# Optimization experiments

Measured on AMD Instinct MI355X. Metric: run time of the kernel, lower is better.

## Reference

```python
import jax, jax.numpy as jnp
import numpy as np

B, S, H = 4, 2048, 1024  # batch, seq, hidden


def setup_inputs() -> dict:
    key = jax.random.key(0)
    kq, kk, kv = jax.random.split(key, 3)
    return {
        "Q": jax.random.normal(kq, (B, S, H), dtype=jnp.float32),
        "K": jax.random.normal(kk, (B, S, H), dtype=jnp.float32),
        "V": jax.random.normal(kv, (B, S, H), dtype=jnp.float32),
    }


def reference(Q, K, V):
    # Phase of rfft along hidden dim -> [B, S, F], F = H//2 + 1
    q_fft = jnp.fft.rfft(Q, axis=-1)
    k_fft = jnp.fft.rfft(K, axis=-1)
    q_phase = jnp.arctan2(q_fft.imag, q_fft.real)
    k_phase = jnp.arctan2(k_fft.imag, k_fft.real)
    n_freqs = q_phase.shape[-1]
    # mean_f cos(qp_i - kp_j) = (cos(qp) @ cos(kp)^T + sin(qp) @ sin(kp)^T) / F
    # Avoids materializing the [B,S,S,F] phase_diff tensor; math is identical.
    align = (
        jnp.einsum("bif,bjf->bij", jnp.cos(q_phase), jnp.cos(k_phase))
        + jnp.einsum("bif,bjf->bij", jnp.sin(q_phase), jnp.sin(k_phase))
    ) / n_freqs
    scores = align + 1.0
    weights = jax.nn.softmax(scores, axis=-1)  # [B, S, S]
    output = jnp.einsum("bij,bjh->bih", weights, V)  # [B, S, H]
    return output, weights
```

## Files before the change

### kernel.cpp

```cpp
#include <hip/hip_runtime.h>
#include <hip/hip_bf16.h>
#include <math.h>

#define Bb 4
#define Ss 2048
#define Hh 1024
#define Ff 513
#define FEAT 1026
#define KP2 1088

typedef __attribute__((ext_vector_type(8))) short bf16x8;
typedef __attribute__((ext_vector_type(4))) float f32x4;

typedef const __attribute__((address_space(1))) void GVoid;
typedef __attribute__((address_space(3))) void LVoid;

#define PADI(i) ((i) + ((i) >> 4))

__device__ __forceinline__ float2 cmul(float2 a, float2 b) {
  return make_float2(a.x * b.x - a.y * b.y, a.x * b.y + a.y * b.x);
}

__device__ __forceinline__ unsigned short bf16bits(float x) {
  __hip_bfloat16 h = __float2bfloat16(x);
  return *reinterpret_cast<unsigned short*>(&h);
}

__device__ __forceinline__ bf16x8 lds_read_b128(const short* p) {
  bf16x8 r;
  asm volatile("ds_read_b128 %0, %1"
               : "=&v"(r)
               : "v"((const __attribute__((address_space(3))) short*)p));
  return r;
}

__global__ __launch_bounds__(256) void fft_phase_kernel(
    const float* __restrict__ Q, const float* __restrict__ Kin,
    __hip_bfloat16* __restrict__ FQ, __hip_bfloat16* __restrict__ FK) {
  const int row = blockIdx.x;
  const float* qs = Q   + (size_t)row * Hh;
  const float* ks = Kin + (size_t)row * Hh;
  __hip_bfloat16* fq = FQ + (size_t)row * KP2;
  __hip_bfloat16* fk = FK + (size_t)row * KP2;

  __shared__ float2 data[PADI(1023) + 1];
  __shared__ float2 tw[1024];
  const int tid = threadIdx.x;

#pragma unroll
  for (int e = 0; e < 4; ++e) {
    const int m = tid + e * 256;
    float s, c;
    sincosf(-6.283185307179586f * (float)m * (1.0f / 1024.0f), &s, &c);
    tw[m] = make_float2(c, s);
  }
#pragma unroll
  for (int e = 0; e < 4; ++e) {
    const int n = tid + e * 256;
    const int r4 = ((n & 3) << 8) | (((n >> 2) & 3) << 6) | (((n >> 4) & 3) << 4)
                 | (((n >> 6) & 3) << 2) | ((n >> 8) & 3);
    data[PADI(r4)] = make_float2(qs[n], ks[n]);
  }
  __syncthreads();

  int quarter = 1, step = 256;
  for (int s = 0; s < 5; ++s) {
    const int j = tid & (quarter - 1);
    const int pos = 4 * tid - 3 * j;
    const float2 x0 = data[PADI(pos)];
    const float2 x1 = data[PADI(pos + quarter)];
    const float2 x2 = data[PADI(pos + 2 * quarter)];
    const float2 x3 = data[PADI(pos + 3 * quarter)];
    const int e1 = j * step;
    const float2 a1 = cmul(x1, tw[e1]);
    const float2 a2 = cmul(x2, tw[2 * e1]);
    const float2 a3 = cmul(x3, tw[3 * e1]);
    const float2 t0 = make_float2(x0.x + a2.x, x0.y + a2.y);
    const float2 t1 = make_float2(x0.x - a2.x, x0.y - a2.y);
    const float2 t2 = make_float2(a1.x + a3.x, a1.y + a3.y);
    const float2 t3 = make_float2(a1.x - a3.x, a1.y - a3.y);
    data[PADI(pos)]               = make_float2(t0.x + t2.x, t0.y + t2.y);
    data[PADI(pos + quarter)]     = make_float2(t1.x + t3.y, t1.y - t3.x);
    data[PADI(pos + 2 * quarter)] = make_float2(t0.x - t2.x, t0.y - t2.y);
    data[PADI(pos + 3 * quarter)] = make_float2(t1.x - t3.y, t1.y + t3.x);
    __syncthreads();
    quarter <<= 2; step >>= 2;
  }

  for (int f = tid; f <= 512; f += 256) {
    const float2 z1 = data[PADI(f)];
    const float2 z2 = data[PADI((1024 - f) & 1023)];
    const float qr = z1.x + z2.x, qi = z1.y - z2.y;
    const float kr = z1.y + z2.y, ki = z2.x - z1.x;
    float qc, qsn, kc, ksn;
    const float qm2 = qr * qr + qi * qi;
    if (qm2 > 1e-30f) { const float iv = rsqrtf(qm2); qc = qr * iv; qsn = qi * iv; }
    else              { qc = 1.0f; qsn = 0.0f; }
    const float km2 = kr * kr + ki * ki;
    if (km2 > 1e-30f) { const float iv = rsqrtf(km2); kc = kr * iv; ksn = ki * iv; }
    else              { kc = 1.0f; ksn = 0.0f; }
    fq[f] = __float2bfloat16(qc); fq[Ff + f] = __float2bfloat16(qsn);
    fk[f] = __float2bfloat16(kc); fk[Ff + f] = __float2bfloat16(ksn);
  }
  for (int p = FEAT + tid; p < KP2; p += 256) {
    fq[p] = __float2bfloat16(0.0f);
    fk[p] = __float2bfloat16(0.0f);
  }
}

__global__ __launch_bounds__(256) void vt_kernel(
    const float* __restrict__ V, __hip_bfloat16* __restrict__ Vt) {
  const int b = blockIdx.z;
  const int h0 = blockIdx.x * 32;
  const int s0 = blockIdx.y * 32;
  __shared__ float t[32][33];
  const int tid = threadIdx.x;
  const int c = tid & 31;
  const int r8 = tid >> 5;
  const float* Vb = V + (size_t)b * Ss * Hh;
#pragma unroll
  for (int e = 0; e < 4; ++e) {
    const int r = r8 + e * 8;
    t[r][c] = Vb[(size_t)(s0 + r) * Hh + h0 + c];
  }
  __syncthreads();
  __hip_bfloat16* O = Vt + (size_t)b * Hh * Ss;
#pragma unroll
  for (int e = 0; e < 4; ++e) {
    const int hh = r8 + e * 8;
    O[(size_t)(h0 + hh) * Ss + s0 + c] = __float2bfloat16(t[c][hh]);
  }
}

template<int K, int LDA, int LDB, int LDC, int EPI, int BNT>
__global__ __launch_bounds__(512, 2) void gemm256(
    const __hip_bfloat16* __restrict__ Ag, const __hip_bfloat16* __restrict__ Bg,
    float* __restrict__ Cg, size_t strA, size_t strB, size_t strC) {
  constexpr int nt = K / 64;
  constexpr int NW = BNT / 64;
  constexpr int LB = BNT / 128;
  const int b = blockIdx.z;
  const int i0 = blockIdx.y * 256;
  const int j0 = blockIdx.x * BNT;
  const char* Ab = (const char*)(Ag + (size_t)b * strA);
  const char* Bp = (const char*)(Bg + (size_t)b * strB);
  float* C = Cg + (size_t)b * strC;

  __shared__ short As[2][16384];
  __shared__ short Bs[2][BNT * 64];

  const int tid = threadIdx.x;
  const int lane = tid & 63;
  const int w  = tid >> 6;
  const int wm = w >> 2;
  const int wn = w & 3;
  const int lr = lane & 15;
  const int lc = lane >> 4;

  f32x4 acc[8][NW];
#pragma unroll
  for (int m = 0; m < 8; ++m)
#pragma unroll
    for (int n = 0; n < NW; ++n)
      acc[m][n] = (f32x4){0.0f, 0.0f, 0.0f, 0.0f};

#define BAR() __builtin_amdgcn_s_barrier()

#define SA(dd, tt, kh)                                                                   \
  do {                                                                                   \
    _Pragma("unroll")                                                                    \
    for (int ii = 0; ii < 2; ++ii) {                                                     \
      const int g = w * 2 + ii;                                                          \
      __builtin_amdgcn_global_load_lds(                                                  \
          (GVoid*)(Ab + (size_t)(i0 + g * 16 + lr) * (LDA * 2) + (size_t)(tt) * 128 +    \
                   (kh) * 64 + lc * 16),                                                 \
          (LVoid*)&As[dd][(g * 2 + (kh)) * 512], 16, 0, 0);                              \
    }                                                                                    \
  } while (0)
#define SB(dd, tt, kh)                                                                   \
  do {                                                                                   \
    _Pragma("unroll")                                                                    \
    for (int ii = 0; ii < LB; ++ii) {                                                    \
      const int g = w * LB + ii;                                                         \
      __builtin_amdgcn_global_load_lds(                                                  \
          (GVoid*)(Bp + (size_t)(j0 + g * 16 + lr) * (LDB * 2) + (size_t)(tt) * 128 +    \
                   (kh) * 64 + lc * 16),                                                 \
          (LVoid*)&Bs[dd][(g * 2 + (kh)) * 512], 16, 0, 0);                              \
    }                                                                                    \
  } while (0)
#define RA(dd, mh, kh)                                                                   \
  _Pragma("unroll")                                                                      \
  for (int mi = 0; mi < 4; ++mi)                                                         \
    af[mi] = lds_read_b128(                                                              \
        &As[dd][(((wm * 8 + (mh) * 4 + mi) * 2 + (kh)) * 4 + lc) * 128 + lr * 8]);
#define RB(dd, kh)                                                                       \
  _Pragma("unroll")                                                                      \
  for (int ni = 0; ni < NW; ++ni)                                                        \
    bf[ni] = lds_read_b128(                                                              \
        &Bs[dd][(((wn * NW + ni) * 2 + (kh)) * 4 + lc) * 128 + lr * 8]);
#define MM(mh)                                                                           \
  asm volatile("s_waitcnt lgkmcnt(0)");                                                  \
  __builtin_amdgcn_sched_barrier(0);                                                     \
  __builtin_amdgcn_s_setprio(1);                                                         \
  _Pragma("unroll")                                                                      \
  for (int mi = 0; mi < 4; ++mi)                                                         \
    _Pragma("unroll")                                                                    \
    for (int ni = 0; ni < NW; ++ni)                                                      \
      acc[(mh) * 4 + mi][ni] =                                                           \
          __builtin_amdgcn_mfma_f32_16x16x32_bf16(af[mi], bf[ni], acc[(mh) * 4 + mi][ni], 0, 0, 0); \
  __builtin_amdgcn_s_setprio(0);                                                         \
  __builtin_amdgcn_sched_barrier(0);

  SA(0, 0, 0); SA(0, 0, 1); SB(0, 0, 0); SB(0, 0, 1);
  SA(1, 1, 0); SA(1, 1, 1); SB(1, 1, 0); SB(1, 1, 1);
  if constexpr (LB == 2) asm volatile("s_waitcnt vmcnt(8)");
  else                   asm volatile("s_waitcnt vmcnt(6)");
  BAR();

  for (int t = 0; t < nt; ++t) {
    const int d = t & 1;
    bf16x8 af[4], bf[NW];

    RA(d, 0, 0); RB(d, 0);
    if (t >= 1 && t + 1 < nt) SA(d ^ 1, t + 1, 1);
    BAR();
    MM(0);
    BAR();

    RA(d, 1, 0);
    if (t + 2 < nt) SB(d, t + 2, 0);
    BAR();
    MM(1);
    BAR();

    RA(d, 0, 1); RB(d, 1);
    if (t + 2 < nt) SA(d, t + 2, 0);
    BAR();
    MM(0);
    BAR();

    RA(d, 1, 1);
    if (t + 2 < nt) SB(d, t + 2, 1);
    BAR();
    MM(1);
    if (t + 2 < nt) {
      if constexpr (LB == 2) asm volatile("s_waitcnt vmcnt(6)");
      else                   asm volatile("s_waitcnt vmcnt(4)");
    } else {
      asm volatile("s_waitcnt vmcnt(0)");
    }
    BAR();
  }
#undef SA
#undef SB
#undef RA
#undef RB
#undef MM
#undef BAR

#pragma unroll
  for (int m = 0; m < 8; ++m) {
    const int ib = i0 + wm * 128 + m * 16 + lc * 4;
#pragma unroll
    for (int n = 0; n < NW; ++n) {
      const int j = j0 + wn * (BNT / 4) + n * 16 + lr;
#pragma unroll
      for (int r = 0; r < 4; ++r) {
        float v = acc[m][n][r];
        if (EPI == 0) v = v * (1.0f / 513.0f);
        C[(size_t)(ib + r) * LDC + j] = v;
      }
    }
  }
}

__global__ __launch_bounds__(256) void softmax_kernel(
    float* __restrict__ W, __hip_bfloat16* __restrict__ Wb) {
  const size_t row = blockIdx.x;
  float* p = W + row * (size_t)Ss;
  __hip_bfloat16* pb = Wb + row * (size_t)Ss;
  const int tid = threadIdx.x;
  __shared__ float red[4];

  const float4* p4 = (const float4*)p;
  const float4 a = p4[2 * tid];
  const float4 bq = p4[2 * tid + 1];
  float v[8] = {a.x, a.y, a.z, a.w, bq.x, bq.y, bq.z, bq.w};

  float m = v[0];
#pragma unroll
  for (int e = 1; e < 8; ++e) m = fmaxf(m, v[e]);
#pragma unroll
  for (int off = 32; off > 0; off >>= 1) m = fmaxf(m, __shfl_xor(m, off, 64));
  if ((tid & 63) == 0) red[tid >> 6] = m;
  __syncthreads();
  m = fmaxf(fmaxf(red[0], red[1]), fmaxf(red[2], red[3]));

  float sum = 0.0f;
#pragma unroll
  for (int e = 0; e < 8; ++e) { v[e] = __expf(v[e] - m); sum += v[e]; }
#pragma unroll
  for (int off = 32; off > 0; off >>= 1) sum += __shfl_xor(sum, off, 64);
  __syncthreads();
  if ((tid & 63) == 0) red[tid >> 6] = sum;
  __syncthreads();
  sum = red[0] + red[1] + red[2] + red[3];

  const float rs = 1.0f / sum;
#pragma unroll
  for (int e = 0; e < 8; ++e) v[e] *= rs;

  float4* o4 = (float4*)p;
  o4[2 * tid]     = make_float4(v[0], v[1], v[2], v[3]);
  o4[2 * tid + 1] = make_float4(v[4], v[5], v[6], v[7]);

  bf16x8 ob;
#pragma unroll
  for (int e = 0; e < 8; ++e) ob[e] = (short)bf16bits(v[e]);
  *(bf16x8*)&pb[8 * tid] = ob;
}

extern "C" void kernel_launch(void* const* d_in, const int* in_sizes, int n_in,
                              void* d_out, int out_size, void* d_ws, size_t ws_size,
                              hipStream_t stream) {
  const float* Q = (const float*)d_in[0];
  const float* K = (const float*)d_in[1];
  const float* V = (const float*)d_in[2];

  float* out     = (float*)d_out;
  float* weights = out + (size_t)Bb * Ss * Hh;

  __hip_bfloat16* FQb = (__hip_bfloat16*)d_ws;
  __hip_bfloat16* FKb = FQb + (size_t)Bb * Ss * KP2;
  __hip_bfloat16* Vtb = FKb + (size_t)Bb * Ss * KP2;
  __hip_bfloat16* Wb  = (__hip_bfloat16*)d_ws;

  hipLaunchKernelGGL(fft_phase_kernel, dim3(Bb * Ss), dim3(256), 0, stream,
                     Q, K, FQb, FKb);
  hipLaunchKernelGGL(vt_kernel, dim3(Hh / 32, Ss / 32, Bb), dim3(256), 0, stream,
                     V, Vtb);
  hipLaunchKernelGGL((gemm256<KP2, KP2, KP2, Ss, 0, 256>), dim3(Ss / 256, Ss / 256, Bb),
                     dim3(512), 0, stream, FQb, FKb, weights,
                     (size_t)Ss * KP2, (size_t)Ss * KP2, (size_t)Ss * Ss);
  hipLaunchKernelGGL(softmax_kernel, dim3(Bb * Ss), dim3(256), 0, stream,
                     weights, Wb);
  hipLaunchKernelGGL((gemm256<Ss, Ss, Ss, Hh, 1, 128>), dim3(Hh / 128, Ss / 256, Bb),
                     dim3(512), 0, stream, Wb, Vtb, out,
                     (size_t)Ss * Ss, (size_t)Hh * Ss, (size_t)Ss * Hh);
}
```

Measured before the change: 169.6 us.

## Switch GEMMs to 32x32x16 MFMA with new LDS layout and XCD-aware block swizzle

Rewrites the bf16 GEMM kernel to use 32x32x16 MFMA instructions instead of 16x16x32. The LDS tile layout and the global-to-LDS load mapping change to match the new operand fragments. The tile shape moves from fixed BM=256 to a templated BM with BN=256, and the second GEMM's grid is reshaped to match. A workgroup-index swizzle spreads consecutive blocks across the 8 XCDs. The larger MFMA is meant to raise tensor throughput per LDS read, at the cost of new layout and waitcnt logic that could be wrong or cause bank conflicts.

```diff
diff --git a/kernel.cpp b/kernel.cpp
--- a/kernel.cpp
+++ b/kernel.cpp
@@ -11,6 +11,7 @@
 
 typedef __attribute__((ext_vector_type(8))) short bf16x8;
 typedef __attribute__((ext_vector_type(4))) float f32x4;
+typedef __attribute__((ext_vector_type(16))) float f32x16;
 
 typedef const __attribute__((address_space(1))) void GVoid;
 typedef __attribute__((address_space(3))) void LVoid;
@@ -132,94 +133,113 @@
   }
 }
 
-template<int K, int LDA, int LDB, int LDC, int EPI, int BNT>
-__global__ __launch_bounds__(512, 2) void gemm256(
+template<int K, int LDA, int LDB, int LDC, int EPI, int BMT>
+__global__ __launch_bounds__(512, 2) void gemm32(
     const __hip_bfloat16* __restrict__ Ag, const __hip_bfloat16* __restrict__ Bg,
     float* __restrict__ Cg, size_t strA, size_t strB, size_t strC) {
-  constexpr int nt = K / 64;
-  constexpr int NW = BNT / 64;
-  constexpr int LB = BNT / 128;
-  const int b = blockIdx.z;
-  const int i0 = blockIdx.y * 256;
-  const int j0 = blockIdx.x * BNT;
-  const char* Ab = (const char*)(Ag + (size_t)b * strA);
-  const char* Bp = (const char*)(Bg + (size_t)b * strB);
-  float* C = Cg + (size_t)b * strC;
-
-  __shared__ short As[2][16384];
-  __shared__ short Bs[2][BNT * 64];
+  constexpr int nt  = K / 64;
+  constexpr int MF  = BMT / 64;
+  constexpr int MPH = MF / 2;
+  constexpr int SAW = MPH;
+
+  const int gx = gridDim.x, gy = gridDim.y;
+  const int nwg = gx * gy * (int)gridDim.z;
+  int f = ((int)blockIdx.z * gy + (int)blockIdx.y) * gx + (int)blockIdx.x;
+  f = (f & 7) * (nwg >> 3) + (f >> 3);
+  const int bx = f % gx; f /= gx;
+  const int by = f % gy;
+  const int bz = f / gy;
+
+  const int i0 = by * BMT;
+  const int j0 = bx * 256;
+  const char* Ab = (const char*)(Ag + (size_t)bz * strA);
+  const char* Bp = (const char*)(Bg + (size_t)bz * strB);
+  float* C = Cg + (size_t)bz * strC;
+
+  __shared__ short As[2][BMT * 64];
+  __shared__ short Bs[2][256 * 64];
 
   const int tid = threadIdx.x;
   const int lane = tid & 63;
   const int w  = tid >> 6;
   const int wm = w >> 2;
   const int wn = w & 3;
-  const int lr = lane & 15;
-  const int lc = lane >> 4;
-
-  f32x4 acc[8][NW];
-#pragma unroll
-  for (int m = 0; m < 8; ++m)
-#pragma unroll
-    for (int n = 0; n < NW; ++n)
-      acc[m][n] = (f32x4){0.0f, 0.0f, 0.0f, 0.0f};
+
+  f32x16 acc[MF][2];
+#pragma unroll
+  for (int mi = 0; mi < MF; ++mi)
+#pragma unroll
+    for (int ni = 0; ni < 2; ++ni)
+#pragma unroll
+      for (int r = 0; r < 16; ++r) acc[mi][ni][r] = 0.0f;
 
 #define BAR() __builtin_amdgcn_s_barrier()
 
 #define SA(dd, tt, kh)                                                                   \
   do {                                                                                   \
     _Pragma("unroll")                                                                    \
-    for (int ii = 0; ii < 2; ++ii) {                                                     \
-      const int g = w * 2 + ii;                                                          \
+    for (int ii = 0; ii < SAW; ++ii) {                                                   \
+      const int f_ = w * SAW + ii;                                                       \
+      const int rg_ = f_ >> 1;                                                           \
+      const int kc_ = 2 * (kh) + (f_ & 1);                                               \
       __builtin_amdgcn_global_load_lds(                                                  \
-          (GVoid*)(Ab + (size_t)(i0 + g * 16 + lr) * (LDA * 2) + (size_t)(tt) * 128 +    \
-                   (kh) * 64 + lc * 16),                                                 \
-          (LVoid*)&As[dd][(g * 2 + (kh)) * 512], 16, 0, 0);                              \
+          (GVoid*)(Ab + (size_t)(i0 + rg_ * 32 + (lane & 31)) * (LDA * 2) +              \
+                   (size_t)(tt) * 128 + kc_ * 32 + (lane >> 5) * 16),                    \
+          (LVoid*)&As[dd][(rg_ * 4 + kc_) * 512], 16, 0, 0);                             \
     }                                                                                    \
   } while (0)
 #define SB(dd, tt, kh)                                                                   \
   do {                                                                                   \
     _Pragma("unroll")                                                                    \
-    for (int ii = 0; ii < LB; ++ii) {                                                    \
-      const int g = w * LB + ii;                                                         \
-      __builtin_amdgcn_global_load_lds(                                                  \
-          (GVoid*)(Bp + (size_t)(j0 + g * 16 + lr) * (LDB * 2) + (size_t)(tt) * 128 +    \
-                   (kh) * 64 + lc * 16),                                                 \
-          (LVoid*)&Bs[dd][(g * 2 + (kh)) * 512], 16, 0, 0);                              \
+    for (int ii = 0; ii < 2; ++ii) {                                                     \
+      const int f_ = w * 2 + ii;                                                         \
+      const int rg_ = f_ >> 1;                                                           \
+      const int kc_ = 2 * (kh) + (f_ & 1);                                               \
+      __builtin_amdgcn_global_lo\
+ad_lds(                                                                                  \
+          (GVoid*)(Bp + (size_t)(j0 + rg_ * 32 + (lane & 31)) * (LDB * 2) +              \
+                   (size_t)(tt) * 128 + kc_ * 32 + (lane >> 5) * 16),                    \
+          (LVoid*)&Bs[dd][(rg_ * 4 + kc_) * 512], 16, 0, 0);                             \
     }                                                                                    \
   } while (0)
 #define RA(dd, mh, kh)                                                                   \
   _Pragma("unroll")                                                                      \
-  for (int mi = 0; mi < 4; ++mi)                                                         \
-    af[mi] = lds_read_b128(                                                              \
-        &As[dd][(((wm * 8 + (mh) * 4 + mi) * 2 + (kh)) * 4 + lc) * 128 + lr * 8]);
+  for (int mi = 0; mi < MPH; ++mi)                                                       \
+    _Pragma("unroll")                                                                    \
+    for (int kb = 0; kb < 2; ++kb)                                                       \
+      af[mi][kb] = lds_read_b128(                                                        \
+          &As[dd][((wm * MF + (mh) * MPH + mi) * 4 + 2 * (kh) + kb) * 512 + lane * 8]);
 #define RB(dd, kh)                                                                       \
   _Pragma("unroll")                                                                      \
-  for (int ni = 0; ni < NW; ++ni)                                                        \
-    bf[ni] = lds_read_b128(                                                              \
-        &Bs[dd][(((wn * NW + ni) * 2 + (kh)) * 4 + lc) * 128 + lr * 8]);
+  for (int ni = 0; ni < 2; ++ni)                                                         \
+    _Pragma("unroll")                                                                    \
+    for (int kb = 0; kb < 2; ++kb)                                                       \
+      bf[ni][kb] = lds_read_b128(                                                        \
+          &Bs[dd][((wn * 2 + ni) * 4 + 2 * (kh) + kb) * 512 + lane * 8]);
 #define MM(mh)                                                                           \
   asm volatile("s_waitcnt lgkmcnt(0)");                                                  \
   __builtin_amdgcn_sched_barrier(0);                                                     \
   __builtin_amdgcn_s_setprio(1);                                                         \
   _Pragma("unroll")                                                                      \
-  for (int mi = 0; mi < 4; ++mi)                                                         \
-    _Pragma("unroll")                                                                    \
-    for (int ni = 0; ni < NW; ++ni)                                                      \
-      acc[(mh) * 4 + mi][ni] =                                                           \
-          __builtin_amdgcn_mfma_f32_16x16x32_bf16(af[mi], bf[ni], acc[(mh) * 4 + mi][ni], 0, 0, 0); \
+  for (int mi = 0; mi < MPH; ++mi)                                                       \
+    _Pragma("unroll")                                                                    \
+    for (int ni = 0; ni < 2; ++ni)                                                       \
+      _Pragma("unroll")                                                                  \
+      for (int kb = 0; kb < 2; ++kb)                                                     \
+        acc[(mh) * MPH + mi][ni] = __builtin_amdgcn_mfma_f32_32x32x16_bf16(              \
+            af[mi][kb], bf[ni][kb], acc[(mh) * MPH + mi][ni], 0, 0, 0);                  \
   __builtin_amdgcn_s_setprio(0);                                                         \
   __builtin_amdgcn_sched_barrier(0);
 
   SA(0, 0, 0); SA(0, 0, 1); SB(0, 0, 0); SB(0, 0, 1);
   SA(1, 1, 0); SA(1, 1, 1); SB(1, 1, 0); SB(1, 1, 1);
-  if constexpr (LB == 2) asm volatile("s_waitcnt vmcnt(8)");
-  else                   asm volatile("s_waitcnt vmcnt(6)");
+  if constexpr (SAW == 2) asm volatile("s_waitcnt vmcnt(8)");
+  else                    asm volatile("s_waitcnt vmcnt(6)");
   BAR();
 
   for (int t = 0; t < nt; ++t) {
     const int d = t & 1;
-    bf16x8 af[4], bf[NW];
+    bf16x8 af[MPH][2], bf[2][2];
 
     RA(d, 0, 0); RB(d, 0);
     if (t >= 1 && t + 1 < nt) SA(d ^ 1, t + 1, 1);
@@ -244,8 +264,8 @@
     BAR();
     MM(1);
     if (t + 2 < nt) {
-      if constexpr (LB == 2) asm volatile("s_waitcnt vmcnt(6)");
-      else                   asm volatile("s_waitcnt vmcnt(4)");
+      if constexpr (SAW == 2) asm volatile("s_waitcnt vmcnt(6)");
+      else                    asm volatile("s_waitcnt vmcnt(5)");
     } else {
       asm volatile("s_waitcnt vmcnt(0)");
     }
@@ -258,17 +278,20 @@
 #undef MM
 #undef BAR
 
-#pragma unroll
-  for (int m = 0; m < 8; ++m) {
-    const int ib = i0 + wm * 128 + m * 16 + lc * 4;
-#pragma unroll
-    for (int n = 0; n < NW; ++n) {
-      const int j = j0 + wn * (BNT / 4) + n * 16 + lr;
-#pragma unroll
-      for (int r = 0; r < 4; ++r) {
-        float v = acc[m][n][r];
-        if (EPI == 0) v = v * (1.0f / 513.0f);
-        C[(size_t)(ib + r) * LDC + j] = v;
+  const int col = lane & 31;
+  const int rbase = (lane >> 5) * 4;
+#pragma unroll
+  for (int mi = 0; mi < MF; ++mi) {
+#pragma unroll
+    for (int ni = 0; ni < 2; ++ni) {
+#pragma unroll
+      for (int r = 0; r < 16; ++r) {
+        const int row = (r & 3) + 8 * (r >> 2) + rbase;
+        const int i = i0 + wm * (MF * 32) + mi * 32 + row;
+        const int j = j0 + wn * 64 + ni * 32 + col;
+        float v = acc[mi][ni][r];
+        if (EPI == 0) v *= (1.0f / 513.0f);
+        C[(size_t)i * LDC + j] = v;
       }
     }
   }
@@ -339,12 +362,12 @@
                      Q, K, FQb, FKb);
   hipLaunchKernelGGL(vt_kernel, dim3(Hh / 32, Ss / 32, Bb), dim3(256), 0, stream,
                      V, Vtb);
-  hipLaunchKernelGGL((gemm256<KP2, KP2, KP2, Ss, 0, 256>), dim3(Ss / 256, Ss / 256, Bb),
+  hipLaunchKernelGGL((gemm32<KP2, KP2, KP2, Ss, 0, 256>), dim3(Ss / 256, Ss / 256, Bb),
                      dim3(512), 0, stream, FQb, FKb, weights,
                      (size_t)Ss * KP2, (size_t)Ss * KP2, (size_t)Ss * Ss);
   hipLaunchKernelGGL(softmax_kernel, dim3(Bb * Ss), dim3(256), 0, stream,
                      weights, Wb);
-  hipLaunchKernelGGL((gemm256<Ss, Ss, Ss, Hh, 1, 128>), dim3(Hh / 128, Ss / 256, Bb),
+  hipLaunchKernelGGL((gemm32<Ss, Ss, Ss, Hh, 1, 128>), dim3(Hh / 256, Ss / 128, Bb),
                      dim3(512), 0, stream, Wb, Vtb, out,
                      (size_t)Ss * Ss, (size_t)Hh * Ss, (size_t)Ss * Hh);
 }
```

Result: no change. 169.3 us (-0.2%).
